# Performance work log

Hardware: AMD Instinct MI355X
Metric: run time of the kernel (lower is better)

The kernel has to match this reference:

```python
import jax, jax.numpy as jnp
import numpy as np

B, S, D = 2, 2048, 1024
H, DK, DV = 16, 64, 64
MASKED = True


def setup_inputs() -> dict:
    key = jax.random.key(0)
    ks = jax.random.split(key, 12)
    s = 0.02
    inp = {
        "Q": jax.random.normal(ks[0], (B, S, D), jnp.float32),
        "K": jax.random.normal(ks[1], (B, S, D), jnp.float32),
        "V": jax.random.normal(ks[2], (B, S, D), jnp.float32),
        "pad_mask": jax.random.randint(ks[3], (B, S), 0, 2, jnp.int32),
        "Wq": jax.random.normal(ks[4], (D, H * DK), jnp.float32) * s,
        "bq": jnp.zeros((H * DK,), jnp.float32),
        "Wk": jax.random.normal(ks[5], (D, H * DK), jnp.float32) * s,
        "bk": jnp.zeros((H * DK,), jnp.float32),
        "Wv": jax.random.normal(ks[6], (D, H * DV), jnp.float32) * s,
        "bv": jnp.zeros((H * DV,), jnp.float32),
        "Wo": jax.random.normal(ks[7], (H * DV, D), jnp.float32) * s,
        "bo": jnp.zeros((D,), jnp.float32),
    }
    return inp


def _split(x):
    # [B,S,H*d] -> [B,H,S,d]
    b, s, _ = x.shape
    return x.reshape(b, s, H, -1).transpose(0, 2, 1, 3)


def reference(Q, K, V, pad_mask, Wq, bq, Wk, bk, Wv, bv, Wo, bo):
    q = _split(Q @ Wq + bq)  # [B,H,S,DK]
    k = _split(K @ Wk + bk)  # [B,H,S,DK]
    v = _split(V @ Wv + bv)  # [B,H,S,DV]

    scores = jnp.einsum("bhqd,bhkd->bhqk", q, k) / np.sqrt(DK)
    mask = pad_mask[:, None, None, :].astype(jnp.float32)  # [B,1,1,S]
    if MASKED:
        causal = jnp.triu(jnp.ones((S, S), jnp.float32), k=1)[None, None]
        mask = ((mask + causal) > 0).astype(jnp.float32)
    scores = scores - 1e9 * mask

    attn = jax.nn.softmax(scores, axis=-1)
    out = jnp.einsum("bhqk,bhkd->bhqd", attn, v)  # [B,H,S,DV]
    out = out.transpose(0, 2, 1, 3).reshape(B, S, H * DV)
    return out @ Wo + bo
```

## Files before the change

kernel.cpp:

```cpp
#include <hip/hip_runtime.h>

typedef unsigned short u16;
typedef unsigned int u32;

typedef __attribute__((ext_vector_type(8))) short bfrag;
typedef __attribute__((ext_vector_type(4))) float f32x4;
typedef __attribute__((ext_vector_type(8))) u16 u16x8;
typedef __attribute__((ext_vector_type(4))) u16 u16x4;

constexpr int S = 2048;
constexpr int HN = 16;
constexpr float QSCALE = 0.18033688011112042f;
constexpr float NBIG   = -1.442695e9f;

__device__ __forceinline__ u16 f2b(float f) {
  u32 u = __builtin_bit_cast(u32, f);
  return (u16)((u + 0x7FFFu + ((u >> 16) & 1u)) >> 16);
}
__device__ __forceinline__ float b2f(u16 v) {
  u32 u = (u32)v << 16;
  return __builtin_bit_cast(float, u);
}
__device__ __forceinline__ u32 cvtpk(float lo, float hi) {
  u32 d;
  asm("v_cvt_pk_bf16_f32 %0, %1, %2" : "=v"(d) : "v"(lo), "v"(hi));
  return d;
}
__device__ __forceinline__ float fexp2(float x) { return __builtin_amdgcn_exp2f(x); }

__device__ __forceinline__ f32x4 mfma16(bfrag a, bfrag b, f32x4 c) {
  return __builtin_amdgcn_mfma_f32_16x16x32_bf16(a, b, c, 0, 0, 0);
}

__device__ __forceinline__ void gload_lds16(const void* g, void* l) {
  __builtin_amdgcn_global_load_lds(
      (const __attribute__((address_space(1))) u32*)g,
      (__attribute__((address_space(3))) u32*)l, 16, 0, 0);
}

__global__ __launch_bounds__(256) void wtrans_kernel(
    const float* __restrict__ W0, const float* __restrict__ W1,
    const float* __restrict__ W2, const float* __restrict__ W3,
    u16* __restrict__ ws,
    const int* __restrict__ pad, u16* __restrict__ idxc, u16* __restrict__ posT,
    int* __restrict__ eqt, float* __restrict__ colsumg)
{
  __shared__ u16 tile[64 * 65];
  const int t = threadIdx.x;

  if (blockIdx.z == 4) {
    if (blockIdx.y != 0 || blockIdx.x >= 2) return;
    int* wtot = (int*)tile;
    int* cntS = (int*)tile + 4;
    const int b = blockIdx.x;
    const int lane = t & 63, w = t >> 6;
    for (int i = t; i < 1024; i += 256) colsumg[b * 1024 + i] = 0.f;
    int4 p0 = *(const int4*)&pad[b * 2048 + t * 8];
    int4 p1 = *(const int4*)&pad[b * 2048 + t * 8 + 4];
    int u[8] = {p0.x == 0, p0.y == 0, p0.z == 0, p0.w == 0,
                p1.x == 0, p1.y == 0, p1.z == 0, p1.w == 0};
    int ps[8], run = 0;
#pragma unroll
    for (int j = 0; j < 8; ++j) { run += u[j]; ps[j] = run; }
    int sc = run;
#pragma unroll
    for (int o = 1; o < 64; o <<= 1) {
      int v = __shfl_up(sc, o);
      if (lane >= o) sc += v;
    }
    if (lane == 63) wtot[w] = sc;
    __syncthreads();
    int base = 0;
#pragma unroll
    for (int i = 0; i < 4; ++i) if (i < w) base += wtot[i];
    int excl = base + sc - run;
#pragma unroll
    for (int j = 0; j < 8; ++j)
      if (u[j]) idxc[b * 2048 + excl + ps[j] - 1] = (u16)(t * 8 + j);
    if ((t & 7) == 7) eqt[b * 32 + (t >> 3)] = base + sc;
    if (t == 255) *cntS = base + sc;
    __syncthreads();
    const int cnt = *cntS;
#pragma unroll
    for (int j = 0; j < 8; ++j) {
      int e = t * 8 + j;
      int pv = u[j] ? (excl + ps[j] - 1) : (cnt + e - excl - ps[j]);
      posT[b * 2048 + e] = (u16)pv;
    }
    for (int j = cnt + t; j < 2048; j += 256) idxc[b * 2048 + j] = 0x7FFF;
    return;
  }

  const float* W = blockIdx.z == 0 ? W0 : blockIdx.z == 1 ? W1 : blockIdx.z == 2 ? W2 : W3;
  const float sc = blockIdx.z == 0 ? QSCALE : 1.0f;
  u16* WT = ws + (size_t)blockIdx.z * (1u << 20);
  const int k0 = blockIdx.y * 64, n0 = blockIdx.x * 64;
#pragma unroll
  for (int i = 0; i < 4; ++i) {
    int idx = i * 256 + t;
    int r = idx >> 4, c4 = (idx & 15) * 4;
    float4 v = *(const float4*)&W[(size_t)(k0 + r) * 1024 + n0 + c4];
    tile[r * 65 + c4 + 0] = f2b(v.x * sc);
    tile[r * 65 + c4 + 1] = f2b(v.y * sc);
    tile[r * 65 + c4 + 2] = f2b(v.z * sc);
    tile[r * 65 + c4 + 3] = f2b(v.w * sc);
  }
  __syncthreads();
#pragma unroll
  for (int i = 0; i < 2; ++i) {
    int idx = i * 256 + t;
    int n = idx >> 3, k8 = (idx & 7) * 8;
    u16x8 o;
#pragma unroll
    for (int j = 0; j < 8; ++j) o[j] = tile[(k8 + j) * 65 + n];
    *(u16x8*)&WT[(size_t)(n0 + n) * 1024 + k0 + k8] = o;
  }
}

__global__ __launch_bounds__(256) void cvt_kernel(
    const float* __restrict__ A0, const float* __restrict__ A1,
    const float* __restrict__ A2, const u16* __restrict__ posT,
    u16* __restrict__ outbase)
{
  const int z = blockIdx.y;
  const float* A = z == 0 ? A0 : z == 1 ? A1 : A2;
  u16* dst = outbase + (size_t)z * (4u << 20);
  const int t = threadIdx.x;
  const int row = blockIdx.x * 2 + (t >> 7);
  const int col = (t & 127) * 8;
  int drow = row;
  if (z == 1) {
    int b = row >> 11;
    drow = b * 2048 + posT[row];
  }
  const float* src = &A[(size_t)row * 1024 + col];
  float4 v0 = *(const float4*)src;
  float4 v1 = *(const float4*)(src + 4);
  union { u32 w[4]; u16x8 v; } o;
  o.w[0] = cvtpk(v0.x, v0.y); o.w[1] = cvtpk(v0.z, v0.w);
  o.w[2] = cvtpk(v1.x, v1.y); o.w[3] = cvtpk(v1.z, v1.w);
  *(u16x8*)&dst[(size_t)drow * 1024 + col] = o.v;
}

__global__ __launch_bounds__(256) void vgather_kernel(
    const u16* __restrict__ vb, const u16* __restrict__ idxc, u16* __restrict__ vTc)
{
  __shared__ u16 tile[64 * 65];
  const int ti = blockIdx.x, bh = blockIdx.y, b = bh >> 4;
  const int t = threadIdx.x;
#pragma unroll
  for (int i = 0; i < 2; ++i) {
    int idx = i * 256 + t;
    int r = idx >> 3, c8 = (idx & 7) * 8;
    int o = idxc[b * 2048 + ti * 64 + r];
    u16x8 in = {};
    if (o != 0x7FFF) in = *(const u16x8*)&vb[((size_t)bh * 2048 + o) * 64 + c8];
#pragma unroll
    for (int j = 0; j < 8; ++j) tile[r * 65 + c8 + j] = in[j];
  }
  __syncthreads();
#pragma unroll
  for (int i = 0; i < 2; ++i) {
    int idx = i * 256 + t;
    int dv = idx >> 3, s8 = (idx & 7) * 8;
    u16x8 o_;
#pragma unroll
    for (int j = 0; j < 8; ++j) o_[j] = tile[(s8 + j) * 65 + dv];
    int a = s8 >> 5, bb = (s8 >> 4) & 1, cc = (s8 >> 3) & 1;
    int s0l = a * 32 + cc * 16 + bb * 4;
    int x = (dv & 7) << 3;
    u16x4 lo = {o_[0], o_[1], o_[2], o_[3]};
    u16x4 hi = {o_[4], o_[5], o_[6], o_[7]};
    size_t rowbase = ((size_t)bh * 64 + dv) * S + ti * 64;
    *(u16x4*)&vTc[rowbase + (s0l ^ x)] = lo;
    *(u16x4*)&vTc[rowbase + ((s0l + 8) ^ x)] = hi;
  }
}

template <int CMODE>
__device__ __forceinline__ void gemm_core(
    u16* As, u16* Bs,
    const u16* __restrict__ A, const u16* __restrict__ Bt,
    const float* __restrict__ bias, void* __restrict__ Cout,
    int N, int K, int bn, int bm, float bscale,
    int kswz, float* __restrict__ csum)
{
  const int tid = threadIdx.x;
  const int wid = tid >> 6, lane = tid & 63;
  const int g = lane >> 4, c = lane & 15;
  const int wr = wid >> 1, wc = wid & 1;

  f32x4 acc[4][2] = {};

  const int nkt = K >> 6;
  for (int kt = 0; kt < nkt; ++kt) {
#pragma unroll
    for (int p = 0; p < 4; ++p) {
      int off = (p * 4 + wid) * 1024 + (lane << 4);
      int row = off >> 7, colb = off & 127;
      gload_lds16(&A[(size_t)(bm * 128 + row) * K + kt * 64 +
                     ((colb ^ ((row & 7) << 4)) >> 1)],
                  (char*)As + (p * 4 + wid) * 1024);
    }
#pragma unroll
    for (int p = 0; p < 2; ++p) {
      int off = (p * 4 + wid) * 1024 + (lane << 4);
      int row = off >> 7, colb = off & 127;
      gload_lds16(&Bt[(size_t)(bn * 64 + row) * K + kt * 64 +
                      ((colb ^ ((row & 7) << 4)) >> 1)],
                  (char*)Bs + (p * 4 + wid) * 1024);
    }
    __syncthreads();

#pragma unroll
    for (int ks = 0; ks < 2; ++ks) {
      bfrag af[4], bf[2];
#pragma unroll
      for (int mi = 0; mi < 4; ++mi) {
        int row = wr * 64 + mi * 16 + c;
        af[mi] = *(const bfrag*)&As[row * 64 + ((ks * 32 + g * 8) ^ ((row & 7) << 3))];
      }
#pragma unroll
      for (int ni = 0; ni < 2; ++ni) {
        int row = wc * 32 + ni * 16 + c;
        bf[ni] = *(const bfrag*)&Bs[row * 64 + ((ks * 32 + g * 8) ^ ((row & 7) << 3))];
      }
#pragma unroll
      for (int mi = 0; mi < 4; ++mi)
#pragma unroll
        for (int ni = 0; ni < 2; ++ni)
          acc[mi][ni] = mfma16(af[mi], bf[ni], acc[mi][ni]);
    }
    __syncthreads();
  }

  float colacc[2] = {0.f, 0.f};
#pragma unroll
  for (int mi = 0; mi < 4; ++mi) {
#pragma unroll
    for (int ni = 0; ni < 2; ++ni) {
#pragma unroll
      for (int j = 0; j < 4; ++j) {
        int rowg = bm * 128 + wr * 64 + mi * 16 + g * 4 + j;
        int colg = bn * 64 + wc * 32 + ni * 16 + c;
        float val = fmaf(bias[colg], bscale, acc[mi][ni][j]);
        if (CMODE == 0) {
          int b = rowg >> 11, s = rowg & (S - 1);
          int h = colg >> 6, d = colg & 63;
          if (kswz) d ^= (s & 7) << 3;
          if (csum) colacc[ni] += val;
          ((u16*)Cout)[((size_t)((b * HN + h) * S + s)) * 64 + d] = f2b(val);
        } else {
          ((float*)Cout)[(size_t)rowg * N + colg] = val;
        }
      }
    }
  }
  if (CMODE == 0 && csum) {
#pragma unroll
    for (int ni = 0; ni < 2; ++ni) {
      float s_ = colacc[ni];
      s_ += __shfl_xor(s_, 16);
      s_ += __shfl_xor(s_, 32);
      if (lane < 16) {
        int colg = bn * 64 + wc * 32 + ni * 16 + c;
        int b = (bm * 128) >> 11;
        atomicAdd(&csum[b * 1024 + colg], s_);
      }
    }
  }
}

__global__ __launch_bounds__(256) void qkv_gemm(
    const u16* __restrict__ Abase, const u16* __restrict__ WTbase,
    const float* __restrict__ b0, const float* __restrict__ b1, const float* __restrict__ b2,
    u16* __restrict__ qb, u16* __restrict__ kc, u16* __restrict__ vb,
    const int* __restrict__ eqt, float* __restrict__ colsumg)
{
  __shared__ __align__(16) u16 As[128 * 64];
  __shared__ __align__(16) u16 Bs[64 * 64];
  const int bid = blockIdx.x;
  const int l = (bid & 7) * 192 + (bid >> 3);
  const int z = l >> 9, rem = l & 511, bm = rem >> 4, bn = rem & 15;
  if (z == 1) {
    int b_ = (bm * 128) >> 11;
    int cnt_ = eqt[b_ * 32 + 31];
    if (((bm * 128) & 2047) >= cnt_) return;
  }
  const u16* A = Abase + (size_t)z * (4u << 20);
  const u16* Bt = WTbase + (size_t)z * (1u << 20);
  const float* bias = z == 0 ? b0 : z == 1 ? b1 : b2;
  u16* C = z == 0 ? qb : z == 1 ? kc : vb;
  gemm_core<0>(As, Bs, A, Bt, bias, C, 1024, 1024, bn, bm,
               z == 0 ? QSCALE : 1.0f,
               z == 1 ? 1 : 0,
               z == 2 ? colsumg : nullptr);
}

__global__ __launch_bounds__(256) void out_gemm(
    const u16* __restrict__ Av, const u16* __restrict__ Bt,
    const float* __restrict__ bias, void* __restrict__ Cout)
{
  __shared__ __align__(16) u16 As[128 * 64];
  __shared__ __align__(16) u16 Bs[64 * 64];
  const int bid = blockIdx.x;
  const int l = (bid & 7) * 64 + (bid >> 3);
  const int bm = l >> 4, bn = l & 15;
  gemm_core<1>(As, Bs, Av, Bt, bias, Cout, 1024, 1024, bn, bm, 1.0f,
               0, nullptr);
}

__global__ __launch_bounds__(256) void attn_kernel(
    const u16* __restrict__ q, const u16* __restrict__ kc,
    const u16* __restrict__ vTc, const u16* __restrict__ idxc,
    const int* __restrict__ eqt, const float* __restrict__ colsumg,
    u16* __restrict__ ao)
{
  __shared__ __align__(16) u16 Ks[2][64 * 64];
  __shared__ __align__(16) u16 Vs[2][64 * 64];

  const int tid = threadIdx.x;
  const int wid = tid >> 6, lane = tid & 63;
  const int g = lane >> 4, c = lane & 15;
  const int i = blockIdx.x;
  const int qt = 31 - (i >> 5);
  const int bh = i & 31;
  const int b = bh >> 4, h = bh & 15;

  const u16* idxb = idxc + b * 2048;
  const int ecnt = eqt[b * 32 + qt];
  const int nt = (ecnt + 63) >> 6;
  const int fz = idxb[0];
  const int qbasew = qt * 64 + wid * 16;
  const int qrow = qbasew + c;

  bfrag qf[2];
#pragma unroll
  for (int ks = 0; ks < 2; ++ks)
    qf[ks] = *(const bfrag*)&q[((size_t)bh * S + qrow) * 64 + ks * 32 + g * 8];

  float m = -3.0e38f, lsum = 0.f;
  f32x4 acc[4] = {};

  const size_t kbase = (size_t)bh * S * 64;
  const size_t vbase = (size_t)bh * 64 * S;
  const int sb = wid * 2048 + (lane << 4);
  const int sb2 = sb + 1024;

#define STAGE(buf, t)                                                              \
  do {                                                                             \
    gload_lds16(&kc[kbase + (size_t)(t) * 4096 + (sb >> 1)],                       \
                (char*)Ks[buf] + wid * 2048);                                      \
    gload_lds16(&kc[kbase + (size_t)(t) * 4096 + (sb2 >> 1)],                      \
                (char*)Ks[buf] + wid * 2048 + 1024);                               \
    gload_lds16(&vTc[vbase + (size_t)(sb >> 7) * S + (t) * 64 + ((sb & 127) >> 1)],\
                (char*)Vs[buf] + wid * 2048);                                      \
    gload_lds16(&vTc[vbase + (size_t)(sb2 >> 7) * S + (t) * 64 + ((sb2 & 127) >> 1)],\
                (char*)Vs[buf] + wid * 2048 + 1024);                               \
  } while (0)

  if (nt > 0) {
    STAGE(0, 0);
    __syncthreads();

    int cur = 0;
    for (int t = 0; t < nt; ++t) {
      if (t + 1 < nt) { STAGE(cur ^ 1, t + 1); }

      f32x4 sc[4] = {};
      __builtin_amdgcn_s_setprio(1);
#pragma unroll
      for (int ks = 0; ks < 2; ++ks)
#pragma unroll
        for (int nf = 0; nf < 4; ++nf) {
          int row = nf * 16 + c;
          bfrag kf = *(const bfrag*)&Ks[cur][row * 64 + ((ks * 32 + g * 8) ^ ((row & 7) << 3))];
          sc[nf] = mfma16(kf, qf[ks], sc[nf]);
        }
      __builtin_amdgcn_s_setprio(0);

      float sval[4][4];
#pragma unroll
      for (int nf = 0; nf < 4; ++nf)
#pragma unroll
        for (int r = 0; r < 4; ++r) sval[nf][r] = sc[nf][r];

      if ((int)idxb[t * 64 + 63] > qbasew) {
#pragma unroll
        for (int nf = 0; nf < 4; ++nf)
#pragma unroll
          for (int r = 0; r < 4; ++r) {
            int ov = idxb[t * 64 + nf * 16 + g * 4 + r];
            if (ov > qrow) sval[nf][r] = NBIG;
          }
      }

      float pm = sval[0][0];
#pragma unroll
      for (int nf = 0; nf < 4; ++nf)
#pragma unroll
        for (int r = 0; r < 4; ++r) pm = fmaxf(pm, sval[nf][r]);
      pm = fmaxf(pm, __shfl_xor(pm, 16));
      pm = fmaxf(pm, __shfl_xor(pm, 32));
      if (!__all(pm - m <= 11.5416f)) {
        float mn = fmaxf(m, pm);
        float fac = fexp2(m - mn);
        lsum *= fac;
#pragma unroll
        for (int nf = 0; nf < 4; ++nf)
#pragma unroll
          for (int j = 0; j < 4; ++j) acc[nf][j] *= fac;
        m = mn;
      }
      float p16v[4][4];
      float rs = 0.f;
#pragma unroll
      for (int nf = 0; nf < 4; ++nf)
#pragma unroll
        for (int r = 0; r < 4; ++r) {
          float pv = fexp2(sval[nf][r] - m);
          p16v[nf][r] = pv;
          rs += pv;
        }
      rs += __shfl_xor(rs, 16);
      rs += __shfl_xor(rs, 32);
      lsum += rs;

      bfrag pa[2];
#pragma unroll
      for (int ks = 0; ks < 2; ++ks) {
        union { u32 w[4]; bfrag f; } pu;
#pragma unroll
        for (int tt = 0; tt < 4; ++tt)
          pu.w[tt] = cvtpk(p16v[2 * ks + (tt >> 1)][2 * (tt & 1)],
                           p16v[2 * ks + (tt >> 1)][2 * (tt & 1) + 1]);
        pa[ks] = pu.f;
      }

      __builtin_amdgcn_s_setprio(1);
#pragma unroll
      for (int ks = 0; ks < 2; ++ks)
#pragma unroll
        for (int nf = 0; nf < 4; ++nf) {
          int row = nf * 16 + c;
          bfrag vf = *(const bfrag*)&Vs[cur][row * 64 + ((ks * 32 + g * 8) ^ ((row & 7) << 3))];
          acc[nf] = mfma16(vf, pa[ks], acc[nf]);
        }
      __builtin_amdgcn_s_setprio(0);

      __syncthreads();
      cur ^= 1;
    }
  }
#undef STAGE

  const float inv = 1.f / lsum;
#pragma unroll
  for (int nf = 0; nf < 4; ++nf) {
    u16x4 ov;
    if (qrow < fz) {
#pragma unroll
      for (int j = 0; j < 4; ++j)
        ov[j] = f2b(colsumg[bh * 64 + nf * 16 + g * 4 + j] * (1.f / 2048.f));
    } else {
#pragma unroll
      for (int j = 0; j < 4; ++j) ov[j] = f2b(acc[nf][j] * inv);
    }
    *(u16x4*)&ao[((size_t)b * S + qrow) * 1024 + h * 64 + nf * 16 + g * 4] = ov;
  }
}

extern "C" void kernel_launch(void* const* d_in, const int* in_sizes, int n_in,
                              void* d_out, int out_size, void* d_ws, size_t ws_size,
                              hipStream_t stream)
{
  const float* Q  = (const float*)d_in[0];
  const float* Kk = (const float*)d_in[1];
  const float* V  = (const float*)d_in[2];
  const int* pad  = (const int*)d_in[3];
  const float* Wq = (const float*)d_in[4];
  const float* bq = (const float*)d_in[5];
  const float* Wk = (const float*)d_in[6];
  const float* bk = (const float*)d_in[7];
  const float* Wv = (const float*)d_in[8];
  const float* bv = (const float*)d_in[9];
  const float* Wo = (const float*)d_in[10];
  const float* bo = (const float*)d_in[11];

  u16* ws  = (u16*)d_ws;
  u16* WoT = ws + 3 * (size_t)(1u << 20);
  u16* qb  = ws + 4 * (size_t)(1u << 20);
  u16* kc  = ws + 8 * (size_t)(1u << 20);
  u16* vb  = ws + 12 * (size_t)(1u << 20);
  u16* vTc = ws + 16 * (size_t)(1u << 20);
  u16* Abf = ws + 20 * (size_t)(1u << 20);
  u16* tab = ws + 32 * (size_t)(1u << 20);
  float* colsumg = (float*)tab;
  u16* idxc = tab + 4096;
  u16* posT = tab + 8192;
  int* eqt  = (int*)(tab + 12288);
  u16* ao   = vb;

  wtrans_kernel<<<dim3(16, 16, 5), 256, 0, stream>>>(Wq, Wk, Wv, Wo, ws,
                                                     pad, idxc, posT, eqt, colsumg);
  cvt_kernel<<<dim3(2048, 3), 256, 0, stream>>>(Q, Kk, V, posT, Abf);
  qkv_gemm<<<1536, 256, 0, stream>>>(Abf, ws, bq, bk, bv, qb, kc, vb, eqt, colsumg);
  vgather_kernel<<<dim3(32, 32), 256, 0, stream>>>(vb, idxc, vTc);
  attn_kernel<<<1024, 256, 0, stream>>>(qb, kc, vTc, idxc, eqt, colsumg, ao);
  out_gemm<<<512, 256, 0, stream>>>(ao, WoT, bo, d_out);
}
```

Measured before the change: 102.8 us.

## Fuse V gather-transpose into QKV GEMM epilogue, drop vgather kernel

The V projection GEMM now writes its output directly in the transposed, compacted, swizzled vTc layout, using posT to map each row to its compacted position. This removes the separate vgather kernel launch and the write and re-read of the intermediate vb buffer. In exchange the V epilogue does scattered 2-byte stores with stride S, which may coalesce poorly. The column-sum accumulation moves into the new epilogue mode.

```diff
diff --git a/kernel.cpp b/kernel.cpp
--- a/kernel.cpp
+++ b/kernel.cpp
@@ -142,48 +142,13 @@
   *(u16x8*)&dst[(size_t)drow * 1024 + col] = o.v;
 }
 
-__global__ __launch_bounds__(256) void vgather_kernel(
-    const u16* __restrict__ vb, const u16* __restrict__ idxc, u16* __restrict__ vTc)
-{
-  __shared__ u16 tile[64 * 65];
-  const int ti = blockIdx.x, bh = blockIdx.y, b = bh >> 4;
-  const int t = threadIdx.x;
-#pragma unroll
-  for (int i = 0; i < 2; ++i) {
-    int idx = i * 256 + t;
-    int r = idx >> 3, c8 = (idx & 7) * 8;
-    int o = idxc[b * 2048 + ti * 64 + r];
-    u16x8 in = {};
-    if (o != 0x7FFF) in = *(const u16x8*)&vb[((size_t)bh * 2048 + o) * 64 + c8];
-#pragma unroll
-    for (int j = 0; j < 8; ++j) tile[r * 65 + c8 + j] = in[j];
-  }
-  __syncthreads();
-#pragma unroll
-  for (int i = 0; i < 2; ++i) {
-    int idx = i * 256 + t;
-    int dv = idx >> 3, s8 = (idx & 7) * 8;
-    u16x8 o_;
-#pragma unroll
-    for (int j = 0; j < 8; ++j) o_[j] = tile[(s8 + j) * 65 + dv];
-    int a = s8 >> 5, bb = (s8 >> 4) & 1, cc = (s8 >> 3) & 1;
-    int s0l = a * 32 + cc * 16 + bb * 4;
-    int x = (dv & 7) << 3;
-    u16x4 lo = {o_[0], o_[1], o_[2], o_[3]};
-    u16x4 hi = {o_[4], o_[5], o_[6], o_[7]};
-    size_t rowbase = ((size_t)bh * 64 + dv) * S + ti * 64;
-    *(u16x4*)&vTc[rowbase + (s0l ^ x)] = lo;
-    *(u16x4*)&vTc[rowbase + ((s0l + 8) ^ x)] = hi;
-  }
-}
-
 template <int CMODE>
 __device__ __forceinline__ void gemm_core(
     u16* As, u16* Bs,
     const u16* __restrict__ A, const u16* __restrict__ Bt,
     const float* __restrict__ bias, void* __restrict__ Cout,
     int N, int K, int bn, int bm, float bscale,
-    int kswz, float* __restrict__ csum)
+    int kswz, const u16* __restrict__ posT, float* __restrict__ csum)
 {
   const int tid = threadIdx.x;
   const int wid = tid >> 6, lane = tid & 63;
@@ -248,15 +213,23 @@
           int b = rowg >> 11, s = rowg & (S - 1);
           int h = colg >> 6, d = colg & 63;
           if (kswz) d ^= (s & 7) << 3;
-          if (csum) colacc[ni] += val;
           ((u16*)Cout)[((size_t)((b * HN + h) * S + s)) * 64 + d] = f2b(val);
+        } else if (CMODE == 1) {
+          ((float*)Cout)[(size_t)rowg * N + colg] = val;
         } else {
-          ((float*)Cout)[(size_t)rowg * N + colg] = val;
+          int b = rowg >> 11, s = rowg & (S - 1);
+          int h = colg >> 6, dv = colg & 63;
+          colacc[ni] += val;
+          int ck = posT[(b << 11) | s];
+          int ti = ck >> 6, jl = ck & 63;
+          int slot = (jl & 35) | ((jl & 8) << 1) | ((jl & 4) << 1) | ((jl & 16) >> 2);
+          int colv = slot ^ ((dv & 7) << 3);
+          ((u16*)Cout)[((size_t)((b * HN + h) * 64 + dv)) * S + ti * 64 + colv] = f2b(val);
         }
       }
     }
   }
-  if (CMODE == 0 && csum) {
+  if (CMODE == 2) {
 #pragma unroll
     for (int ni = 0; ni < 2; ++ni) {
       float s_ = colacc[ni];
@@ -274,27 +247,27 @@
 __global__ __launch_bounds__(256) void qkv_gemm(
     const u16* __restrict__ Abase, const u16* __restrict__ WTbase,
     const float* __restrict__ b0, const float* __restrict__ b1, const float* __restrict__ b2,
-    u16* __restrict__ qb, u16* __restrict__ kc, u16* __restrict__ vb,
-    const int* __restrict__ eqt, float* __restrict__ colsumg)
+    u16* __restrict__ qb, u16* __restrict__ kc, u16* __restrict__ vTc,
+    const int* __restrict__ eqt, const u16* __restrict__ posT,
+    float* __restrict__ colsumg)
 {
   __shared__ __align__(16) u16 As[128 * 64];
   __shared__ __align__(16) u16 Bs[64 * 64];
   const int bid = blockIdx.x;
   const int l = (bid & 7) * 192 + (bid >> 3);
   const int z = l >> 9, rem = l & 511, bm = rem >> 4, bn = rem & 15;
-  if (z == 1) {
+  const u16* A = Abase + (size_t)z * (4u << 20);
+  const u16* Bt = WTbase + (size_t)z * (1u << 20);
+  if (z == 0) {
+    gemm_core<0>(As, Bs, A, Bt, b0, qb, 1024, 1024, bn, bm, QSCALE, 0, nullptr, nullptr);
+  } else if (z == 1) {
     int b_ = (bm * 128) >> 11;
     int cnt_ = eqt[b_ * 32 + 31];
     if (((bm * 128) & 2047) >= cnt_) return;
-  }
-  const u16* A = Abase + (size_t)z * (4u << 20);
-  const u16* Bt = WTbase + (size_t)z * (1u << 20);
-  const float* bias = z == 0 ? b0 : z == 1 ? b1 : b2;
-  u16* C = z == 0 ? qb : z == 1 ? kc : vb;
-  gemm_core<0>(As, Bs, A, Bt, bias, C, 1024, 1024, bn, bm,
-               z == 0 ? QSCALE : 1.0f,
-               z == 1 ? 1 : 0,
-               z == 2 ? colsumg : nullptr);
+    gemm_core<0>(As, Bs, A, Bt, b1, kc, 1024, 1024, bn, bm, 1.0f, 1, nullptr, nullptr);
+  } else {
+    gemm_core<2>(As, Bs, A, Bt, b2, vTc, 1024, 1024, bn, bm, 1.0f, 0, posT, colsumg);
+  }
 }
 
 __global__ __launch_bounds__(256) void out_gemm(
@@ -307,7 +280,7 @@
   const int l = (bid & 7) * 64 + (bid >> 3);
   const int bm = l >> 4, bn = l & 15;
   gemm_core<1>(As, Bs, Av, Bt, bias, Cout, 1024, 1024, bn, bm, 1.0f,
-               0, nullptr);
+               0, nullptr, nullptr);
 }
 
 __global__ __launch_bounds__(256) void attn_kernel(
@@ -491,7 +464,7 @@
   u16* WoT = ws + 3 * (size_t)(1u << 20);
   u16* qb  = ws + 4 * (size_t)(1u << 20);
   u16* kc  = ws + 8 * (size_t)(1u << 20);
-  u16* vb  = ws + 12 * (size_t)(1u << 20);
+  u16* ao  = ws + 12 * (size_t)(1u << 20);
   u16* vTc = ws + 16 * (size_t)(1u << 20);
   u16* Abf = ws + 20 * (size_t)(1u << 20);
   u16* tab = ws + 32 * (size_t)(1u << 20);
@@ -499,13 +472,11 @@
   u16* idxc = tab + 4096;
   u16* posT = tab + 8192;
   int* eqt  = (int*)(tab + 12288);
-  u16* ao   = vb;
 
   wtrans_kernel<<<dim3(16, 16, 5), 256, 0, stream>>>(Wq, Wk, Wv, Wo, ws,
                                                      pad, idxc, posT, eqt, colsumg);
   cvt_kernel<<<dim3(2048, 3), 256, 0, stream>>>(Q, Kk, V, posT, Abf);
-  qkv_gemm<<<1536, 256, 0, stream>>>(Abf, ws, bq, bk, bv, qb, kc, vb, eqt, colsumg);
-  vgather_kernel<<<dim3(32, 32), 256, 0, stream>>>(vb, idxc, vTc);
+  qkv_gemm<<<1536, 256, 0, stream>>>(Abf, ws, bq, bk, bv, qb, kc, vTc, eqt, posT, colsumg);
   attn_kernel<<<1024, 256, 0, stream>>>(qb, kc, vTc, idxc, eqt, colsumg, ao);
   out_gemm<<<512, 256, 0, stream>>>(ao, WoT, bo, d_out);
 }
```

New measurement: 119.0 us. 15.8% more time.
